# Performance work log

Hardware: AMD Instinct MI355X
Metric: run time of the kernel (lower is better)

## Reference

```python
import jax, jax.numpy as jnp
import numpy as np

N = 100000
E = 6400000
IN_CH = 128
HID = 5
H1 = 2
OUT = 10
H2 = 1
EPS_BN = 1e-5


def glorot(key, shape):
    fan = shape[0] + shape[-1]
    s = jnp.sqrt(6.0 / fan)
    return jax.random.uniform(key, shape, jnp.float32, -s, s)


def setup_inputs() -> dict:
    key = jax.random.key(0)
    ks = jax.random.split(key, 12)
    x = jax.random.normal(ks[0], (N, IN_CH), jnp.float32)
    edge_index = jax.random.randint(ks[1], (2, E), 0, N, jnp.int64)
    return {
        "x": x,
        "W1": glorot(ks[2], (IN_CH, H1 * HID)),
        "a_src1": glorot(ks[3], (H1, HID)),
        "a_dst1": glorot(ks[4], (H1, HID)),
        "b1": jnp.zeros((H1 * HID,), jnp.float32),
        "gamma1": jnp.ones((H1 * HID,), jnp.float32),
        "beta1": jnp.zeros((H1 * HID,), jnp.float32),
        "W2": glorot(ks[5], (H1 * HID, H2 * OUT)),
        "a_src2": glorot(ks[6], (H2, OUT)),
        "a_dst2": glorot(ks[7], (H2, OUT)),
        "b2": jnp.zeros((OUT,), jnp.float32),
        "edge_index": edge_index,
    }


def gat_conv(x, src, dst, W, a_src, a_dst, bias, heads, out_ch, concat):
    n = x.shape[0]
    h = (x @ W).reshape(n, heads, out_ch)          # [N,H,C]
    alpha_s = (h * a_src).sum(-1)                  # [N,H]
    alpha_d = (h * a_dst).sum(-1)                  # [N,H]
    e = jax.nn.leaky_relu(alpha_s[src] + alpha_d[dst], 0.2)  # [E,H]
    emax = jax.ops.segment_max(e, dst, num_segments=n)
    emax = jnp.where(jnp.isfinite(emax), emax, 0.0)
    ex = jnp.exp(e - jax.lax.stop_gradient(emax)[dst])
    denom = jax.ops.segment_sum(ex, dst, num_segments=n)
    alpha = ex / (denom[dst] + 1e-16)              # edge softmax by target
    msg = h[src] * alpha[..., None]                # [E,H,C]
    out = jax.ops.segment_sum(msg, dst, num_segments=n)
    out = out.reshape(n, heads * out_ch) if concat else out.mean(axis=1)
    return out + bias


def batch_norm(x, gamma, beta):
    mu = x.mean(0)
    var = ((x - mu) ** 2).mean(0)
    return (x - mu) * jax.lax.rsqrt(var + EPS_BN) * gamma + beta


def reference(x, W1, a_src1, a_dst1, b1, gamma1, beta1, W2, a_src2, a_dst2, b2, edge_index):
    n = x.shape[0]
    loop = jnp.arange(n, dtype=edge_index.dtype)   # add_self_loops=True
    src = jnp.concatenate([edge_index[0], loop])
    dst = jnp.concatenate([edge_index[1], loop])
    h = gat_conv(x, src, dst, W1, a_src1, a_dst1, b1, H1, HID, True)
    h = batch_norm(h, gamma1, beta1)
    h = jax.nn.elu(h)
    out = gat_conv(h, src, dst, W2, a_src2, a_dst2, b2, H2, OUT, False)
    return out
```

## Files before the change

### kernel.cpp

```cpp
#include <hip/hip_runtime.h>
#include <hip/hip_fp16.h>
#include <math.h>

#define NN 100000
#define NE 6400000
#define INCH 128
#define BSH 7
#define BW (1 << BSH)
#define NBKT ((NN + BW - 1) / BW)
#define NBP 784
#define BCAP 9216
#define SCAP 6144
#define BIN_CH 8192
#define NAGG (2 * NBKT)
#define BNP2 1600

__device__ inline float pkh(float a, float b) {
  __half2 h = __floats2half2_rn(a, b);
  return __uint_as_float(*reinterpret_cast<unsigned int*>(&h));
}
__device__ inline float2 uph(float f) {
  unsigned int b = __float_as_uint(f);
  __half2 h = *reinterpret_cast<__half2*>(&b);
  return __half22float2(h);
}

__global__ __launch_bounds__(512) void k_count(const int* __restrict__ ei,
                                               int* __restrict__ cntmat) {
  __shared__ int cnt4[4][NBKT];
  int t = threadIdx.x;
  int w = (t >> 6) & 3;
  for (int i = t; i < 4 * NBKT; i += 512) (&cnt4[0][0])[i] = 0;
  __syncthreads();
  int c0 = blockIdx.x * BIN_CH;
  int c1 = c0 + BIN_CH < NE ? c0 + BIN_CH : NE;
  int n4 = (c1 - c0) >> 2;
  const int4* d4 = (const int4*)(ei + NE + c0);
  for (int k = t; k < n4; k += 512) {
    int4 v = d4[k];
    atomicAdd(&cnt4[w][v.x >> BSH], 1);
    atomicAdd(&cnt4[w][v.y >> BSH], 1);
    atomicAdd(&cnt4[w][v.z >> BSH], 1);
    atomicAdd(&cnt4[w][v.w >> BSH], 1);
  }
  __syncthreads();
  for (int b = t; b < NBKT; b += 512)
    cntmat[(size_t)b * NBP + blockIdx.x] =
        cnt4[0][b] + cnt4[1][b] + cnt4[2][b] + cnt4[3][b];
}

__global__ __launch_bounds__(64) void k_scanb(const int* __restrict__ cntmat,
                                              int* __restrict__ basemat,
                                              int* __restrict__ bcnt) {
  int j = blockIdx.x;
  int lane = threadIdx.x;
  int carry = 0;
  for (int i0 = 0; i0 < NBKT; i0 += 64) {
    int i = i0 + lane;
    int v0 = (i < NBKT) ? cntmat[(size_t)j * NBP + i] : 0;
    int v = v0;
#pragma unroll
    for (int off = 1; off < 64; off <<= 1) {
      int u = __shfl_up(v, off, 64);
      if (lane >= off) v += u;
    }
    if (i < NBKT) basemat[(size_t)i * NBP + j] = carry + v - v0;
    carry += __shfl(v, 63, 64);
  }
  if (lane == 0) bcnt[j] = carry;
}

__global__ __launch_bounds__(1024) void k_scatter2(
    const int* __restrict__ ei, const int* __restrict__ cntmat,
    const int* __restrict__ basemat, unsigned int* __restrict__ pairs) {
  __shared__ int offs[NBKT];
  __shared__ int cur[NBKT];
  __shared__ int gbase[NBKT];
  __shared__ int scanp[1024];
  __shared__ unsigned int stage[BIN_CH];
  __shared__ unsigned short sbkt[BIN_CH];
  int t = threadIdx.x;
  int chunk = blockIdx.x;
  int myb0 = t * 4;
  int tots[4];
  int asum = 0;
#pragma unroll
  for (int j = 0; j < 4; j++) {
    int b = myb0 + j;
    int tt = (b < NBKT) ? cntmat[(size_t)b * NBP + chunk] : 0;
    tots[j] = tt;
    asum += tt;
  }
  for (int b = t; b < NBKT; b += 1024)
    gbase[b] = basemat[(size_t)chunk * NBP + b];
  scanp[t] = asum;
  __syncthreads();
  for (int off = 1; off < 1024; off <<= 1) {
    int v = (t >= off) ? scanp[t - off] : 0;
    __syncthreads();
    scanp[t] += v;
    __syncthreads();
  }
  int run = (t == 0) ? 0 : scanp[t - 1];
#pragma unroll
  for (int j = 0; j < 4; j++) {
    int b = myb0 + j;
    if (b < NBKT) {
      offs[b] = run;
      cur[b] = run;
      run += tots[j];
    }
  }
  __syncthreads();
  int c0 = chunk * BIN_CH;
  int c1 = c0 + BIN_CH < NE ? c0 + BIN_CH : NE;
  for (int i = c0 + t; i < c1; i += 1024) {
    int s = ei[i], d = ei[NE + i];
    int bkt = d >> BSH;
    int pos = atomicAdd(&cur[bkt], 1);
    stage[pos] = ((unsigned int)s << BSH) | (unsigned int)(d & (BW - 1));
    sbkt[pos] = (unsigned short)bkt;
  }
  __syncthreads();
  int total = c1 - c0;
  for (int i = t; i < total; i += 1024) {
    unsigned int e = stage[i];
    int b = sbkt[i];
    int gp = gbase[b] + (i - offs[b]);
    if (gp < BCAP) pairs[(size_t)b * BCAP + gp] = e;
  }
}

__global__ __launch_bounds__(1024) void k_sortb(
    const int* __restrict__ bcnt, unsigned int* __restrict__ pairs,
    unsigned int* __restrict__ oc) {
  __shared__ int cnt16[16][BW];
  __shared__ int wb16[16][BW];
  __shared__ int tot[BW];
  __shared__ int scanbuf[BW];
  __shared__ unsigned int sorted[BCAP];
  int t = threadIdx.x;
  int w = t >> 6;
  int b = blockIdx.x;
  int base_n = b << BSH;
  for (int i = t; i < 16 * BW; i += 1024) (&cnt16[0][0])[i] = 0;
  __syncthreads();
  int cntb = bcnt[b];
  cntb = cntb > BCAP ? BCAP : cntb;
  unsigned int* pp = pairs + (size_t)b * BCAP;
  for (int k = t; k < cntb; k += 1024)
    atomicAdd(&cnt16[w][pp[k] & (BW - 1)], 1);
  __syncthreads();
  if (t < BW) {
    int tt = 0;
#pragma unroll
    for (int j = 0; j < 16; j++) tt += cnt16[j][t];
    tot[t] = tt;
    scanbuf[t] = tt;
  }
  __syncthreads();
  for (int step = 1; step < BW; step <<= 1) {
    int v = 0;
    if (t < BW && t >= step) v = scanbuf[t - step];
    __syncthreads();
    if (t < BW) scanbuf[t] += v;
    __syncthreads();
  }
  if (t < BW) {
    int run = scanbuf[t] - tot[t];
    int n = base_n + t;
    if (n < NN) oc[n] = ((unsigned int)run << 16) | (unsigned int)tot[t];
#pragma unroll
    for (int j = 0; j < 16; j++) { wb16[j][t] = run; run += cnt16[j][t]; cnt16[j][t] = 0; }
  }
  __syncthreads();
  for (int k = t; k < cntb; k += 1024) {
    unsigned int e = pp[k];
    int dl = e & (BW - 1);
    int pos = wb16[w][dl] + atomicAdd(&cnt16[w][dl], 1);
    sorted[pos] = e >> BSH;
  }
  __syncthreads();
  for (int k = t; k < cntb; k += 1024) pp[k] = sorted[k];
}

__global__ __launch_bounds__(256) void k_l1_node(
    const float* __restrict__ x, const float* __restrict__ W1,
    const float* __restrict__ a_src1, const float* __restrict__ a_dst1,
    float* __restrict__ h1, float2* __restrict__ ad1) {
  __shared__ float Wt[10 * INCH];
  __shared__ float asw[10], adw[10];
  for (int i = threadIdx.x; i < 10 * INCH; i += blockDim.x) {
    int c = i / 10, k = i - c * 10;
    Wt[k * INCH + c] = W1[i];
  }
  if (threadIdx.x < 10) {
    asw[threadIdx.x] = a_src1[threadIdx.x];
    adw[threadIdx.x] = a_dst1[threadIdx.x];
  }
  __syncthreads();
  int n = blockIdx.x * blockDim.x + threadIdx.x;
  if (n >= NN) return;
  const float4* xr = (const float4*)(x + (size_t)n * INCH);
  const float4* Wt4 = (const float4*)Wt;
  float acc[10];
#pragma unroll
  for (int k = 0; k < 10; k++) acc[k] = 0.f;
#pragma unroll 8
  for (int c4 = 0; c4 < INCH / 4; c4++) {
    float4 xv = xr[c4];
#pragma unroll
    for (int k = 0; k < 10; k++) {
      float4 wv = Wt4[k * (INCH / 4) + c4];
      acc[k] += xv.x * wv.x + xv.y * wv.y + xv.z * wv.z + xv.w * wv.w;
    }
  }
  float s0 = 0.f, s1 = 0.f, d0 = 0.f, d1 = 0.f;
#pragma unroll
  for (int j = 0; j < 5; j++) {
    s0 += acc[j] * asw[j];
    s1 += acc[5 + j] * asw[5 + j];
    d0 += acc[j] * adw[j];
    d1 += acc[5 + j] * adw[5 + j];
  }
  float4* hrow = (float4*)(h1 + (size_t)n * 8);
  hrow[0] = make_float4(pkh(acc[0], acc[1]), pkh(acc[2], acc[3]),
                        pkh(acc[4], 0.f), s0);
  hrow[1] = make_float4(pkh(acc[5], acc[6]), pkh(acc[7], acc[8]),
                        pkh(acc[9], 0.f), s1);
  ad1[n] = make_float2(d0, d1);
}

__global__ __launch_bounds__(512, 8) void k_l1_aggs(
    const int* __restrict__ bcnt,
    const unsigned int* __restrict__ sorted_g, const unsigned int* __restrict__ oc,
    const float* __restrict__ h1, const float2* __restrict__ ad1,
    const float* __restrict__ b1, float* __restrict__ g1,
    float* __restrict__ bn_part) {
  __shared__ __align__(16) unsigned int sorted[SCAP];
  __shared__ float biasS[10];
  __shared__ float bn_lds[8 * 20];
  int t = threadIdx.x;
  int w = t >> 6;
  int blk = blockIdx.x;
  int bkt = blk >> 1, sub = blk & 1;
  int base_n = (bkt << BSH) + (sub << 6);
  if (t < 10) biasS[t] = b1[t];
  int cb = bcnt[bkt];
  cb = cb > BCAP ? BCAP : cb;
  int s_lo = 0, s_hi = 0;
  if (base_n < NN) {
    s_lo = (int)(oc[base_n] >> 16);
    int nxt = base_n + 64;
    if (((nxt & (BW - 1)) != 0) && nxt < NN) s_hi = (int)(oc[nxt] >> 16);
    else s_hi = cb;
  }
  int al = s_lo & ~3;
  int slen = s_hi - al;
  slen = slen > SCAP ? SCAP : slen;
  {
    int n4 = (slen + 3) >> 2;
    const uint4* pp4 = (const uint4*)(sorted_g + (size_t)bkt * BCAP + al);
    uint4* s4 = (uint4*)sorted;
    for (int k = t; k < n4; k += 512) s4[k] = pp4[k];
  }
  __syncthreads();
  int lane = t & 63;
  int odd = t & 1;
  int pairIdx = (t >> 1) & 3;
  int ol = (lane & 56) | 1;
  int node = t >> 3;
  int n = base_n + node;
  bool valid = n < NN;
  unsigned int ocv = valid ? oc[n] : 0u;
  int s0i = (int)(ocv >> 16) - al;
  int c = (int)(ocv & 0xffffu);
  int cmax = slen - s0i;
  c = c < cmax ? c : (cmax > 0 ? cmax : 0);
  float2 adn = valid ? ad1[n] : make_float2(0.f, 0.f);
  float ad_h = odd ? adn.y : adn.x;
  float r0 = 0.f, r1 = 0.f, r2 = 0.f, r3 = 0.f, r4 = 0.f, den = 0.f;
  for (int k = pairIdx; k < c; k += 4) {
    int s = (int)sorted[s0i + k];
    const float4* hs = (const float4*)(h1 + (size_t)s * 8);
    float4 rv = hs[odd];
    float e = rv.w + ad_h; e = e > 0.f ? e : 0.2f * e;
    float xv = __expf(e);
    float2 p01 = uph(rv.x), p23 = uph(rv.y);
    float p4 = uph(rv.z).x;
    r0 += xv * p01.x; r1 += xv * p01.y; r2 += xv * p23.x;
    r3 += xv * p23.y; r4 += xv * p4;
    den += xv;
  }
#pragma unroll
  for (int off = 2; off <= 4; off <<= 1) {
    r0 += __shfl_xor(r0, off, 64); r1 += __shfl_xor(r1, off, 64);
    r2 += __shfl_xor(r2, off, 64); r3 += __shfl_xor(r3, off, 64);
    r4 += __shfl_xor(r4, off, 64); den += __shfl_xor(den, off, 64);
  }
  float q0 = __shfl(r0, ol, 64), q1 = __shfl(r1, ol, 64);
  float q2 = __shfl(r2, ol, 64), q3 = __shfl(r3, ol, 64);
  float q4 = __shfl(r4, ol, 64), qden = __shfl(den, ol, 64);
  float v[10];
#pragma unroll
  for (int j = 0; j < 10; j++) v[j] = 0.f;
  if ((t & 7) == 0 && valid) {
    const float4* hs = (const float4*)(h1 + (size_t)n * 8);
    float4 ra = hs[0], rb = hs[1];
    float e0 = ra.w + adn.x; e0 = e0 > 0.f ? e0 : 0.2f * e0;
    float e1 = rb.w + adn.y; e1 = e1 > 0.f ? e1 : 0.2f * e1;
    float x0 = __expf(e0), x1 = __expf(e1);
    float2 h01 = uph(ra.x), h23 = uph(ra.y);
    float h4 = uph(ra.z).x;
    float2 h56 = uph(rb.x), h78 = uph(rb.y);
    float h9 = uph(rb.z).x;
    float a0 = r0 + x0 * h01.x, a1 = r1 + x0 * h01.y;
    float a2 = r2 + x0 * h23.x, a3 = r3 + x0 * h23.y;
    float a4 = r4 + x0 * h4;
    float a5 = q0 + x1 * h56.x, a6 = q1 + x1 * h56.y;
    float a7 = q2 + x1 * h78.x, a8 = q3 + x1 * h78.y;
    float a9 = q4 + x1 * h9;
    float den0 = den + x0, den1 = qden + x1;
    float i0 = 1.f / (den0 + 1e-16f), i1 = 1.f / (den1 + 1e-16f);
    v[0] = a0 * i0 + biasS[0]; v[1] = a1 * i0 + biasS[1];
    v[2] = a2 * i0 + biasS[2]; v[3] = a3 * i0 + biasS[3];
    v[4] = a4 * i0 + biasS[4];
    v[5] = a5 * i1 + biasS[5]; v[6] = a6 * i1 + biasS[6];
    v[7] = a7 * i1 + biasS[7]; v[8] = a8 * i1 + biasS[8];
    v[9] = a9 * i1 + biasS[9];
    float4* gr = (float4*)(g1 + (size_t)n * 12);
    gr[0] = make_float4(v[0], v[1], v[2], v[3]);
    gr[1] = make_float4(v[4], v[5], v[6], v[7]);
    gr[2] = make_float4(v[8], v[9], 0.f, 0.f);
  }
  float bnv[20];
#pragma unroll
  for (int j = 0; j < 10; j++) { bnv[j] = v[j]; bnv[10 + j] = v[j] * v[j]; }
#pragma unroll
  for (int j = 0; j < 20; j++) {
    bnv[j] += __shfl_down(bnv[j], 8, 64);
    bnv[j] += __shfl_down(bnv[j], 16, 64);
    bnv[j] += __shfl_down(bnv[j], 32, 64);
  }
  if ((t & 63) == 0) {
#pragma unroll
    for (int j = 0; j < 20; j++) bn_lds[w * 20 + j] = bnv[j];
  }
  __syncthreads();
  if (t == 0) {
#pragma unroll
    for (int j = 0; j < 20; j++) {
      float acc20 = 0.f;
#pragma unroll
      for (int ww = 0; ww < 8; ww++) acc20 += bn_lds[ww * 20 + j];
      bn_part[j * BNP2 + blk] = acc20;
    }
  }
}

__global__ __launch_bounds__(64) void k_bnred(const float* __restrict__ bn_part,
                                              float* __restrict__ bns) {
  int j = blockIdx.x;
  int lane = threadIdx.x;
  float s = 0.f;
  for (int b = lane; b < NAGG; b += 64) s += bn_part[j * BNP2 + b];
#pragma unroll
  for (int off = 32; off > 0; off >>= 1) s += __shfl_down(s, off, 64);
  if (lane == 0) bns[j] = s;
}

__global__ __launch_bounds__(256) void k_l2_node(
    const float* __restrict__ g1, const float* __restrict__ bns,
    const float* __restrict__ gamma1, const float* __restrict__ beta1,
    const float* __restrict__ W2, const float* __restrict__ a_src2,
    const float* __restrict__ a_dst2, float* __restrict__ h2,
    float* __restrict__ ad2) {
  __shared__ float scale[10], shift[10], W2s[100], a2s[10], a2d[10];
  if (threadIdx.x < 10) {
    int j = threadIdx.x;
    float mu = bns[j] * (1.f / NN);
    float var = bns[10 + j] * (1.f / NN) - mu * mu;
    float rs = rsqrtf(var + 1e-5f);
    scale[j] = rs * gamma1[j];
    shift[j] = beta1[j] - mu * rs * gamma1[j];
    a2s[j] = a_src2[j];
    a2d[j] = a_dst2[j];
  }
  for (int i = threadIdx.x; i < 100; i += blockDim.x) W2s[i] = W2[i];
  __syncthreads();
  int n = blockIdx.x * blockDim.x + threadIdx.x;
  if (n >= NN) return;
  const float4* gr = (const float4*)(g1 + (size_t)n * 12);
  float4 g0 = gr[0], g1v = gr[1], g2 = gr[2];
  float hv[10] = {g0.x, g0.y, g0.z, g0.w, g1v.x, g1v.y, g1v.z, g1v.w, g2.x, g2.y};
#pragma unroll
  for (int j = 0; j < 10; j++) {
    float t = hv[j] * scale[j] + shift[j];
    hv[j] = t > 0.f ? t : expm1f(t);
  }
  float o[10];
#pragma unroll
  for (int k = 0; k < 10; k++) o[k] = 0.f;
#pragma unroll
  for (int c = 0; c < 10; c++) {
#pragma unroll
    for (int k = 0; k < 10; k++) o[k] += hv[c] * W2s[c * 10 + k];
  }
  float ss = 0.f, sd = 0.f;
#pragma unroll
  for (int k = 0; k < 10; k++) { ss += o[k] * a2s[k]; sd += o[k] * a2d[k]; }
  float4* hr = (float4*)(h2 + (size_t)n * 8);
  hr[0] = make_float4(pkh(o[0], o[1]), pkh(o[2], o[3]), pkh(o[4], 0.f), ss);
  hr[1] = make_float4(pkh(o[5], o[6]), pkh(o[7], o[8]), pkh(o[9], 0.f), ss);
  ad2[n] = sd;
}

__global__ __launch_bounds__(512, 8) void k_l2_aggs(
    const int* __restrict__ bcnt,
    const unsigned int* __restrict__ sorted_g, const unsigned int* __restrict__ oc,
    const float* __restrict__ h2, const float* __restrict__ ad2,
    const float* __restrict__ b2, float* __restrict__ out) {
  __shared__ __align__(16) unsigned int sorted[SCAP];
  __shared__ float biasS[10];
  int t = threadIdx.x;
  int blk = blockIdx.x;
  int bkt = blk >> 1, sub = blk & 1;
  int base_n = (bkt << BSH) + (sub << 6);
  if (t < 10) biasS[t] = b2[t];
  int cb = bcnt[bkt];
  cb = cb > BCAP ? BCAP : cb;
  int s_lo = 0, s_hi = 0;
  if (base_n < NN) {
    s_lo = (int)(oc[base_n] >> 16);
    int nxt = base_n + 64;
    if (((nxt & (BW - 1)) != 0) && nxt < NN) s_hi = (int)(oc[nxt] >> 16);
    else s_hi = cb;
  }
  int al = s_lo & ~3;
  int slen = s_hi - al;
  slen = slen > SCAP ? SCAP : slen;
  {
    int n4 = (slen + 3) >> 2;
    const uint4* pp4 = (const uint4*)(sorted_g + (size_t)bkt * BCAP + al);
    uint4* s4 = (uint4*)sorted;
    for (int k = t; k < n4; k += 512) s4[k] = pp4[k];
  }
  __syncthreads();
  int lane = t & 63;
  int odd = t & 1;
  int pairIdx = (t >> 1) & 3;
  int ol = (lane & 56) | 1;
  int node = t >> 3;
  int n = base_n + node;
  bool valid = n < NN;
  unsigned int ocv = valid ? oc[n] : 0u;
  int s0i = (int)(ocv >> 16) - al;
  int c = (int)(ocv & 0xffffu);
  int cmax = slen - s0i;
  c = c < cmax ? c : (cmax > 0 ? cmax : 0);
  float adn = valid ? ad2[n] : 0.f;
  float r0 = 0.f, r1 = 0.f, r2 = 0.f, r3 = 0.f, r4 = 0.f, den = 0.f;
  for (int k = pairIdx; k < c; k += 4) {
    int s = (int)sorted[s0i + k];
    const float4* hs = (const float4*)(h2 + (size_t)s * 8);
    float4 rv = hs[odd];
    float e = rv.w + adn; e = e > 0.f ? e : 0.2f * e;
    float xv = __expf(e);
    float2 p01 = uph(rv.x), p23 = uph(rv.y);
    float p4 = uph(rv.z).x;
    r0 += xv * p01.x; r1 += xv * p01.y; r2 += xv * p23.x;
    r3 += xv * p23.y; r4 += xv * p4;
    den += xv;
  }
#pragma unroll
  for (int off = 2; off <= 4; off <<= 1) {
    r0 += __shfl_xor(r0, off, 64); r1 += __shfl_xor(r1, off, 64);
    r2 += __shfl_xor(r2, off, 64); r3 += __shfl_xor(r3, off, 64);
    r4 += __shfl_xor(r4, off, 64); den += __shfl_xor(den, off, 64);
  }
  float q0 = __shfl(r0, ol, 64), q1 = __shfl(r1, ol, 64);
  float q2 = __shfl(r2, ol, 64), q3 = __shfl(r3, ol, 64);
  float q4 = __shfl(r4, ol, 64);
  if ((t & 7) == 0 && valid) {
    const float4* hs = (const float4*)(h2 + (size_t)n * 8);
    float4 ra = hs[0], rb = hs[1];
    float e = ra.w + adn; e = e > 0.f ? e : 0.2f * e;
    float xv = __expf(e);
    float2 h01 = uph(ra.x), h23 = uph(ra.y);
    float h4 = uph(ra.z).x;
    float2 h56 = uph(rb.x), h78 = uph(rb.y);
    float h9 = uph(rb.z).x;
    float a0 = r0 + xv * h01.x, a1 = r1 + xv * h01.y;
    float a2 = r2 + xv * h23.x, a3 = r3 + xv * h23.y;
    float a4 = r4 + xv * h4;
    float a5 = q0 + xv * h56.x, a6 = q1 + xv * h56.y;
    float a7 = q2 + xv * h78.x, a8 = q3 + xv * h78.y;
    float a9 = q4 + xv * h9;
    float dd = den + xv;
    float inv = 1.f / (dd + 1e-16f);
    float2* orow = (float2*)(out + (size_t)n * 10);
    orow[0] = make_float2(a0 * inv + biasS[0], a1 * inv + biasS[1]);
    orow[1] = make_float2(a2 * inv + biasS[2], a3 * inv + biasS[3]);
    orow[2] = make_float2(a4 * inv + biasS[4], a5 * inv + biasS[5]);
    orow[3] = make_float2(a6 * inv + biasS[6], a7 * inv + biasS[7]);
    orow[4] = make_float2(a8 * inv + biasS[8], a9 * inv + biasS[9]);
  }
}

extern "C" void kernel_launch(void* const* d_in, const int* in_sizes, int n_in,
                              void* d_out, int out_size, void* d_ws, size_t ws_size,
                              hipStream_t stream) {
  const float* x      = (const float*)d_in[0];
  const float* W1     = (const float*)d_in[1];
  const float* a_src1 = (const float*)d_in[2];
  const float* a_dst1 = (const float*)d_in[3];
  const float* b1     = (const float*)d_in[4];
  const float* gamma1 = (const float*)d_in[5];
  const float* beta1  = (const float*)d_in[6];
  const float* W2     = (const float*)d_in[7];
  const float* a_src2 = (const float*)d_in[8];
  const float* a_dst2 = (const float*)d_in[9];
  const float* b2     = (const float*)d_in[10];
  const int*   ei     = (const int*)d_in[11];
  float* out = (float*)d_out;

  int* bcnt = (int*)d_ws;
  unsigned int* pairs = (unsigned int*)d_ws + 1024;
  float* h1 = (float*)(pairs + (size_t)NBKT * BCAP);
  float* ad1 = h1 + (size_t)NN * 8;
  float* g1 = ad1 + (size_t)NN * 2;
  float* h2 = g1 + (size_t)NN * 12;
  float* ad2 = h2 + (size_t)NN * 8;
  float* bn_part = ad2 + NN;
  float* bns = bn_part + 20 * BNP2;
  int* cntmat = (int*)(bns + 20 + 12);
  int* basemat = cntmat + (size_t)NBKT * NBP;
  unsigned int* oc = (unsigned int*)(basemat + (size_t)NBKT * NBP);

  const int B = 256;
  const int gN = (NN + B - 1) / B;
  const int gBin = (NE + BIN_CH - 1) / BIN_CH;

  k_count<<<gBin, 512, 0, stream>>>(ei, cntmat);
  k_scanb<<<NBKT, 64, 0, stream>>>(cntmat, basemat, bcnt);
  k_scatter2<<<gBin, 1024, 0, stream>>>(ei, cntmat, basemat, pairs);
  k_sortb<<<NBKT, 1024, 0, stream>>>(bcnt, pairs, oc);
  k_l1_node<<<gN, B, 0, stream>>>(x, W1, a_src1, a_dst1, h1, (float2*)ad1);
  k_l1_aggs<<<NAGG, 512, 0, stream>>>(bcnt, pairs, oc, h1, (const float2*)ad1,
                                      b1, g1, bn_part);
  k_bnred<<<20, 64, 0, stream>>>(bn_part, bns);
  k_l2_node<<<gN, B, 0, stream>>>(g1, bns, gamma1, beta1, W2, a_src2, a_dst2,
                                  h2, ad2);
  k_l2_aggs<<<NAGG, 512, 0, stream>>>(bcnt, pairs, oc, h2, ad2, b2, out);
}
```

Measured before the change: 310.9 us.

## Vectorize edge loads, use wave-shuffle scan, unroll gather loops four-wide

The scatter kernel now reads edge indices as int4 and replaces the 1024-step shared-memory block scan with a wave-level shuffle scan plus a per-wave sum. The bucket sort kernel reads and writes pairs as uint4. Both aggregation kernels unroll the neighbor gather four times so that four independent row loads are in flight per thread. The aim is fewer memory instructions and barriers and more memory-level parallelism on the latency-bound gathers, at the cost of higher register pressure. The int4 scatter loop drops any tail, which is only safe because the edge count is a multiple of four.

```diff
diff --git a/kernel.cpp b/kernel.cpp
--- a/kernel.cpp
+++ b/kernel.cpp
@@ -76,7 +76,7 @@
   __shared__ int offs[NBKT];
   __shared__ int cur[NBKT];
   __shared__ int gbase[NBKT];
-  __shared__ int scanp[1024];
+  __shared__ int wsum[16];
   __shared__ unsigned int stage[BIN_CH];
   __shared__ unsigned short sbkt[BIN_CH];
   int t = threadIdx.x;
@@ -93,15 +93,19 @@
   }
   for (int b = t; b < NBKT; b += 1024)
     gbase[b] = basemat[(size_t)chunk * NBP + b];
-  scanp[t] = asum;
-  __syncthreads();
-  for (int off = 1; off < 1024; off <<= 1) {
-    int v = (t >= off) ? scanp[t - off] : 0;
-    __syncthreads();
-    scanp[t] += v;
-    __syncthreads();
-  }
-  int run = (t == 0) ? 0 : scanp[t - 1];
+  int lane = t & 63, wv = t >> 6;
+  int v = asum;
+#pragma unroll
+  for (int off = 1; off < 64; off <<= 1) {
+    int u = __shfl_up(v, off, 64);
+    if (lane >= off) v += u;
+  }
+  if (lane == 63) wsum[wv] = v;
+  __syncthreads();
+  int base = 0;
+#pragma unroll
+  for (int j = 0; j < 16; j++) base += (j < wv) ? wsum[j] : 0;
+  int run = base + v - asum;
 #pragma unroll
   for (int j = 0; j < 4; j++) {
     int b = myb0 + j;
@@ -114,12 +118,20 @@
   __syncthreads();
   int c0 = chunk * BIN_CH;
   int c1 = c0 + BIN_CH < NE ? c0 + BIN_CH : NE;
-  for (int i = c0 + t; i < c1; i += 1024) {
-    int s = ei[i], d = ei[NE + i];
-    int bkt = d >> BSH;
-    int pos = atomicAdd(&cur[bkt], 1);
-    stage[pos] = ((unsigned int)s << BSH) | (unsigned int)(d & (BW - 1));
-    sbkt[pos] = (unsigned short)bkt;
+  int n4e = (c1 - c0) >> 2;
+  const int4* sv4 = (const int4*)(ei + c0);
+  const int4* dv4 = (const int4*)(ei + NE + c0);
+  for (int k = t; k < n4e; k += 1024) {
+    int4 ss = sv4[k];
+    int4 dd = dv4[k];
+#pragma unroll
+    for (int j = 0; j < 4; j++) {
+      int s = (&ss.x)[j], d = (&dd.x)[j];
+      int bkt = d >> BSH;
+      int pos = atomicAdd(&cur[bkt], 1);
+      stage[pos] = ((unsigned int)s << BSH) | (unsigned int)(d & (BW - 1));
+      sbkt[pos] = (unsigned short)bkt;
+    }
   }
   __syncthreads();
   int total = c1 - c0;
@@ -148,7 +160,16 @@
   int cntb = bcnt[b];
   cntb = cntb > BCAP ? BCAP : cntb;
   unsigned int* pp = pairs + (size_t)b * BCAP;
-  for (int k = t; k < cntb; k += 1024)
+  const uint4* pp4r = (const uint4*)pp;
+  int n4v = cntb >> 2;
+  for (int k = t; k < n4v; k += 1024) {
+    uint4 e4 = pp4r[k];
+    atomicAdd(&cnt16[w][e4.x & (BW - 1)], 1);
+    atomicAdd(&cnt16[w][e4.y & (BW - 1)], 1);
+    atomicAdd(&cnt16[w][e4.z & (BW - 1)], 1);
+    atomicAdd(&cnt16[w][e4.w & (BW - 1)], 1);
+  }
+  for (int k = (n4v << 2) + t; k < cntb; k += 1024)
     atomicAdd(&cnt16[w][pp[k] & (BW - 1)], 1);
   __syncthreads();
   if (t < BW) {
@@ -174,14 +195,27 @@
     for (int j = 0; j < 16; j++) { wb16[j][t] = run; run += cnt16[j][t]; cnt16[j][t] = 0; }
   }
   __syncthreads();
-  for (int k = t; k < cntb; k += 1024) {
+  for (int k = t; k < n4v; k += 1024) {
+    uint4 e4 = pp4r[k];
+#pragma unroll
+    for (int j = 0; j < 4; j++) {
+      unsigned int e = (&e4.x)[j];
+      int dl = e & (BW - 1);
+      int pos = wb16[w][dl] + atomicAdd(&cnt16[w][dl], 1);
+      sorted[pos] = e >> BSH;
+    }
+  }
+  for (int k = (n4v << 2) + t; k < cntb; k += 1024) {
     unsigned int e = pp[k];
     int dl = e & (BW - 1);
     int pos = wb16[w][dl] + atomicAdd(&cnt16[w][dl], 1);
     sorted[pos] = e >> BSH;
   }
   __syncthreads();
-  for (int k = t; k < cntb; k += 1024) pp[k] = sorted[k];
+  int n4w = (cntb + 3) >> 2;
+  uint4* ppw = (uint4*)pp;
+  const uint4* s4r = (const uint4*)sorted;
+  for (int k = t; k < n4w; k += 1024) ppw[k] = s4r[k];
 }
 
 __global__ __launch_bounds__(256) void k_l1_node(
@@ -230,6 +264,17 @@
                         pkh(acc[9], 0.f), s1);
   ad1[n] = make_float2(d0, d1);
 }
+
+#define GAT_PROC(rv)                                            \
+  do {                                                          \
+    float e_ = (rv).w + ad_h; e_ = e_ > 0.f ? e_ : 0.2f * e_;   \
+    float x_ = __expf(e_);                                      \
+    float2 p01_ = uph((rv).x), p23_ = uph((rv).y);              \
+    float p4_ = uph((rv).z).x;                                  \
+    r0 += x_ * p01_.x; r1 += x_ * p01_.y; r2 += x_ * p23_.x;    \
+    r3 += x_ * p23_.y; r4 += x_ * p4_;                          \
+    den += x_;                                                  \
+  } while (0)
 
 __global__ __launch_bounds__(512, 8) void k_l1_aggs(
     const int* __restrict__ bcnt,
@@ -280,17 +325,22 @@
   float2 adn = valid ? ad1[n] : make_float2(0.f, 0.f);
   float ad_h = odd ? adn.y : adn.x;
   float r0 = 0.f, r1 = 0.f, r2 = 0.f, r3 = 0.f, r4 = 0.f, den = 0.f;
-  for (int k = pairIdx; k < c; k += 4) {
+  int k = pairIdx;
+  for (; k + 12 < c; k += 16) {
+    int sA = (int)sorted[s0i + k];
+    int sB = (int)sorted[s0i + k + 4];
+    int sC = (int)sorted[s0i + k + 8];
+    int sD = (int)sorted[s0i + k + 12];
+    float4 rvA = ((const float4*)(h1 + (size_t)sA * 8))[odd];
+    float4 rvB = ((const float4*)(h1 + (size_t)sB * 8))[odd];
+    float4 rvC = ((const float4*)(h1 + (size_t)sC * 8))[odd];
+    float4 rvD = ((const float4*)(h1 + (size_t)sD * 8))[odd];
+    GAT_PROC(rvA); GAT_PROC(rvB); GAT_PROC(rvC); GAT_PROC(rvD);
+  }
+  for (; k < c; k += 4) {
     int s = (int)sorted[s0i + k];
-    const float4* hs = (const float4*)(h1 + (size_t)s * 8);
-    float4 rv = hs[odd];
-    float e = rv.w + ad_h; e = e > 0.f ? e : 0.2f * e;
-    float xv = __expf(e);
-    float2 p01 = uph(rv.x), p23 = uph(rv.y);
-    float p4 = uph(rv.z).x;
-    r0 += xv * p01.x; r1 += xv * p01.y; r2 += xv * p23.x;
-    r3 += xv * p23.y; r4 += xv * p4;
-    den += xv;
+    float4 rv = ((const float4*)(h1 + (size_t)s * 8))[odd];
+    GAT_PROC(rv);
   }
 #pragma unroll
   for (int off = 2; off <= 4; off <<= 1) {
@@ -459,18 +509,24 @@
   int cmax = slen - s0i;
   c = c < cmax ? c : (cmax > 0 ? cmax : 0);
   float adn = valid ? ad2[n] : 0.f;
+  float ad_h = adn;
   float r0 = 0.f, r1 = 0.f, r2 = 0.f, r3 = 0.f, r4 = 0.f, den = 0.f;
-  for (int k = pairIdx; k < c; k += 4) {
+  int k = pairIdx;
+  for (; k + 12 < c; k += 16) {
+    int sA = (int)sorted[s0i + k];
+    int sB = (int)sorted[s0i + k + 4];
+    int sC = (int)sorted[s0i + k + 8];
+    int sD = (int)sorted[s0i + k + 12];
+    float4 rvA = ((const float4*)(h2 + (size_t)sA * 8))[odd];
+    float4 rvB = ((const float4*)(h2 + (size_t)sB * 8))[odd];
+    float4 rvC = ((const float4*)(h2 + (size_t)sC * 8))[odd];
+    float4 rvD = ((const float4*)(h2 + (size_t)sD * 8))[odd];
+    GAT_PROC(rvA); GAT_PROC(rvB); GAT_PROC(rvC); GAT_PROC(rvD);
+  }
+  for (; k < c; k += 4) {
     int s = (int)sorted[s0i + k];
-    const float4* hs = (const float4*)(h2 + (size_t)s * 8);
-    float4 rv = hs[odd];
-    float e = rv.w + adn; e = e > 0.f ? e : 0.2f * e;
-    float xv = __expf(e);
-    float2 p01 = uph(rv.x), p23 = uph(rv.y);
-    float p4 = uph(rv.z).x;
-    r0 += xv * p01.x; r1 += xv * p01.y; r2 += xv * p23.x;
-    r3 += xv * p23.y; r4 += xv * p4;
-    den += xv;
+    float4 rv = ((const float4*)(h2 + (size_t)s * 8))[odd];
+    GAT_PROC(rv);
   }
 #pragma unroll
   for (int off = 2; off <= 4; off <<= 1) {
```

Measured after the change: 298.5 us. 1.04x faster.
